# Optimization experiments

Hardware: AMD Instinct MI355X
Metric: run time of the kernel (lower is better)

The kernel has to match this reference:

```python
import jax, jax.numpy as jnp
from jax import lax
import numpy as np

LRELU_SLOPE = 0.1
DILATIONS = (1, 2, 4)
B, C, T = 8, 256, 8192


def pd_indexing(x, d, dilation):
    """Pitch-dependent past/future gather along time.
    x: (B, C, T); d: (B, 1, T) float dilation factors.
    Returns xP, xF: (B, C, T), zero where index is out of range.
    """
    b, c, t_len = x.shape
    t = jnp.arange(t_len, dtype=x.dtype)  # (T,)
    dil = d[:, 0, :] * dilation           # (B, T)
    idxP = jnp.round(t[None, :] - dil).astype(jnp.int32)  # (B, T)
    idxF = jnp.round(t[None, :] + dil).astype(jnp.int32)  # (B, T)
    validP = (idxP >= 0).astype(x.dtype)[:, None, :]        # (B,1,T)
    validF = (idxF < t_len).astype(x.dtype)[:, None, :]
    idxPc = jnp.broadcast_to(jnp.clip(idxP, 0, t_len - 1)[:, None, :], (b, c, t_len))
    idxFc = jnp.broadcast_to(jnp.clip(idxF, 0, t_len - 1)[:, None, :], (b, c, t_len))
    xP = jnp.take_along_axis(x, idxPc, axis=2) * validP
    xF = jnp.take_along_axis(x, idxFc, axis=2) * validF
    return xP, xF


def conv1x1(x, w, bias):
    # x: (B,C,T), w: (O,C), bias: (O,)
    return jnp.einsum('oc,bct->bot', w, x) + bias[None, :, None]


def conv3(x, w, bias):
    # x: (B,C,T), w: (O,C,3), padding=1
    y = lax.conv_general_dilated(x, w, window_strides=(1,), padding=[(1, 1)],
                                 dimension_numbers=('NCH', 'OIH', 'NCH'))
    return y + bias[None, :, None]


def setup_inputs() -> dict:
    key = jax.random.key(0)
    ks = jax.random.split(key, 8)
    x = jax.random.normal(ks[0], (B, C, T), dtype=jnp.float32)
    d = jax.random.uniform(ks[1], (B, 1, T), dtype=jnp.float32, minval=0.0, maxval=16.0)
    n = len(DILATIONS)
    s1 = 1.0 / np.sqrt(C)
    s3 = 1.0 / np.sqrt(3 * C)
    WC = jax.random.normal(ks[2], (n, C, C), dtype=jnp.float32) * s1
    WP = jax.random.normal(ks[3], (n, C, C), dtype=jnp.float32) * s1
    WF = jax.random.normal(ks[4], (n, C, C), dtype=jnp.float32) * s1
    WA = jax.random.normal(ks[5], (n, C, C, 3), dtype=jnp.float32) * s3
    bC = jnp.zeros((n, C), dtype=jnp.float32)
    bP = jnp.zeros((n, C), dtype=jnp.float32)
    bF = jnp.zeros((n, C), dtype=jnp.float32)
    bA = jnp.zeros((n, C), dtype=jnp.float32)
    return {"x": x, "d": d, "WC": WC, "bC": bC, "WP": WP, "bP": bP,
            "WF": WF, "bF": bF, "WA": WA, "bA": bA}


def reference(x, d, WC, bC, WP, bP, WF, bF, WA, bA):
    for i, dilation in enumerate(DILATIONS):
        xt = jax.nn.leaky_relu(x, LRELU_SLOPE)
        xP, xF = pd_indexing(xt, d, dilation)
        xt = conv1x1(xt, WC[i], bC[i]) + conv1x1(xP, WP[i], bP[i]) + conv1x1(xF, WF[i], bF[i])
        xt = jax.nn.leaky_relu(xt, LRELU_SLOPE)
        xt = conv3(xt, WA[i], bA[i])
        x = xt + x
    return x
```

## Files before the change

### kernel.cpp

```cpp
#include <hip/hip_runtime.h>
#include <hip/hip_bf16.h>
#include <cstddef>
#include <cstdint>

constexpr int Bn = 8, Cn = 256, Tn = 8192;
constexpr int NL = 3;
constexpr int Kc = 768;
constexpr float SLOPE = 0.1f;

typedef unsigned short u16;
using bf8   = __attribute__((ext_vector_type(8))) short;
using f32x4 = __attribute__((ext_vector_type(4))) float;

__device__ __forceinline__ float lrelu(float v) { return v > 0.f ? v : SLOPE * v; }
__device__ __forceinline__ u16 f2bf(float f) {
    __hip_bfloat16 h = __float2bfloat16(f);
    return *reinterpret_cast<u16*>(&h);
}

__device__ __forceinline__ void g2l16(const u16* g, u16* l) {
    __builtin_amdgcn_global_load_lds(
        (const __attribute__((address_space(1))) char*)g,
        (__attribute__((address_space(3))) char*)l, 16, 0, 0);
}

__global__ __launch_bounds__(256)
void k_wprep(const float* __restrict__ WC, const float* __restrict__ WP,
             const float* __restrict__ WF, const float* __restrict__ WA,
             const float* __restrict__ bC, const float* __restrict__ bP,
             const float* __restrict__ bF,
             u16* __restrict__ Wcat, u16* __restrict__ WAp, float* __restrict__ bSum,
             u16* __restrict__ zrow)
{
    if (blockIdx.x == 0) zrow[threadIdx.x] = 0;
    const int n1 = NL * Cn * Kc;
    for (int i = blockIdx.x * blockDim.x + threadIdx.x; i < n1;
         i += gridDim.x * blockDim.x) {
        int c = i % Cn;
        int s = (i / Cn) % 3;
        int o = (i / (3 * Cn)) % Cn;
        int l = i / (3 * Cn * Cn);
        size_t src = ((size_t)l * Cn + o) * Cn + c;
        float wc = (s == 0) ? WC[src] : (s == 1) ? WP[src] : WF[src];
        Wcat[i] = f2bf(wc);
        WAp[i] = f2bf(WA[src * 3 + s]);
    }
    for (int i = blockIdx.x * blockDim.x + threadIdx.x; i < NL * Cn;
         i += gridDim.x * blockDim.x)
        bSum[i] = bC[i] + bP[i] + bF[i];
}

__global__ __launch_bounds__(256)
void k_prep(const float* __restrict__ x, u16* __restrict__ xT)
{
    __shared__ float s[64][65];
    const int b = blockIdx.z, c0 = blockIdx.y * 64, t0 = blockIdx.x * 64;
    const int tid = threadIdx.x;
    const float* xb = x + ((size_t)b * Cn + c0) * Tn + t0;

    int tt = tid & 63, c4 = tid >> 6;
    for (int cc = c4; cc < 64; cc += 4)
        s[cc][tt] = xb[(size_t)cc * Tn + tt];
    __syncthreads();

    int ccS = tid & 63, t4 = tid >> 6;
    u16* xTb = xT + ((size_t)b * Tn + t0) * Cn + c0;
    for (int t2 = t4; t2 < 64; t2 += 4)
        xTb[(size_t)t2 * Cn + ccS] = f2bf(lrelu(s[ccS][t2]));
}

__global__ __launch_bounds__(256)
void k_gemm1(const u16* __restrict__ xT, const float* __restrict__ d,
             const u16* __restrict__ Wl, const float* __restrict__ bS,
             float dil, u16* __restrict__ zT, const u16* __restrict__ zrow)
{
    __shared__ u16 sX[128 * 32];
    __shared__ u16 sW[128 * 32];
    __shared__ int sRow[3][128];

    const int tid = threadIdx.x;
    const int b = blockIdx.z;
    const int t0 = blockIdx.x * 128;
    const int o0 = blockIdx.y * 128;

    if (tid < 128) {
        int t = t0 + tid;
        float dv = d[(size_t)b * Tn + t] * dil;
        int ip = (int)rintf((float)t - dv);
        int iF = (int)rintf((float)t + dv);
        sRow[0][tid] = t;
        sRow[1][tid] = (ip >= 0) ? ip : -1;
        sRow[2][tid] = (iF < Tn) ? iF : -1;
    }
    __syncthreads();

    const int srow = tid >> 2;
    const int schunk = (tid & 3) * 8;
    const u16* xTb = xT + (size_t)b * Tn * Cn;

    const u16 *pr0[3], *pr1[3];
    #pragma unroll
    for (int s = 0; s < 3; ++s) {
        int r0 = sRow[s][srow], r1 = sRow[s][srow + 64];
        pr0[s] = (r0 >= 0) ? (xTb + (size_t)r0 * Cn + schunk) : (zrow + schunk);
        pr1[s] = (r1 >= 0) ? (xTb + (size_t)r1 * Cn + schunk) : (zrow + schunk);
    }

    const int lane = tid & 63, wv = tid >> 6;
    const int wm = (wv & 1) * 64;
    const int wn = (wv >> 1) * 64;
    const int lr = lane & 15, quad = lane >> 4;

    f32x4 acc[4][4] = {};

    #pragma unroll
    for (int seg = 0; seg < 3; ++seg) {
        const u16* xr0 = pr0[seg];
        const u16* xr1 = pr1[seg];
        const u16* wp0 = Wl + (size_t)(o0 + srow) * Kc + seg * 256 + schunk;
        const u16* wp1 = wp0 + (size_t)64 * Kc;
        #pragma unroll
        for (int kk = 0; kk < 256; kk += 32) {
            __syncthreads();
            g2l16(wp0 + kk, sW + srow * 32 + schunk);
            g2l16(wp1 + kk, sW + (srow + 64) * 32 + schunk);
            g2l16(xr0 + kk, sX + srow * 32 + schunk);
            g2l16(xr1 + kk, sX + (srow + 64) * 32 + schunk);
            __syncthreads();

            bf8 af[4], bg[4];
            #pragma unroll
            for (int mi = 0; mi < 4; ++mi)
                af[mi] = *(const bf8*)(sX + (wm + mi * 16 + lr) * 32 + quad * 8);
            #pragma unroll
            for (int ni = 0; ni < 4; ++ni)
                bg[ni] = *(const bf8*)(sW + (wn + ni * 16 + lr) * 32 + quad * 8);
            #pragma unroll
            for (int mi = 0; mi < 4; ++mi)
                #pragma unroll
                for (int ni = 0; ni < 4; ++ni)
                    acc[mi][ni] = __builtin_amdgcn_mfma_f32_16x16x32_bf16(
                        af[mi], bg[ni], acc[mi][ni], 0, 0, 0);
        }
    }

    float bias[4];
    #pragma unroll
    for (int ni = 0; ni < 4; ++ni) bias[ni] = bS[o0 + wn + ni * 16 + lr];
    u16* zTb = zT + (size_t)b * Tn * Cn;
    #pragma unroll
    for (int mi = 0; mi < 4; ++mi)
        #pragma unroll
        for (int r = 0; r < 4; ++r) {
            int t = t0 + wm + mi * 16 + quad * 4 + r;
            u16* row = zTb + (size_t)t * Cn + o0 + wn;
            #pragma unroll
            for (int ni = 0; ni < 4; ++ni)
                row[ni * 16 + lr] = f2bf(lrelu(acc[mi][ni][r] + bias[ni]));
        }
}

__global__ __launch_bounds__(256)
void k_gemm2(const u16* __restrict__ zT, const u16* __restrict__ WAl,
             const float* __restrict__ bA, const float* __restrict__ xres,
             float* __restrict__ out, u16* __restrict__ xTn, int writeXT,
             const u16* __restrict__ zrow)
{
    __shared__ u16 smem[128 * 32 * 2];
    u16* sZ = smem;
    u16* sW = smem + 4096;

    const int tid = threadIdx.x;
    const int b = blockIdx.z;
    const int t0 = blockIdx.x * 128;
    const int o0 = blockIdx.y * 128;

    const int srow = tid >> 2;
    const int schunk = (tid & 3) * 8;
    const int lane = tid & 63, wv = tid >> 6;
    const int wo = (wv & 1) * 64;
    const int wt = (wv >> 1) * 64;
    const int lr = lane & 15, quad = lane >> 4;

    f32x4 acc[4][4] = {};
    const u16* zTb = zT + (size_t)b * Tn * Cn;

    #pragma unroll
    for (int tap = 0; tap < 3; ++tap) {
        const int r0 = t0 + srow + tap - 1;
        const int r1 = r0 + 64;
        const u16* zr0 = (r0 >= 0 && r0 < Tn) ? (zTb + (size_t)r0 * Cn + schunk)
                                              : (zrow + schunk);
        const u16* zr1 = (r1 >= 0 && r1 < Tn) ? (zTb + (size_t)r1 * Cn + schunk)
                                              : (zrow + schunk);
        const u16* wp0 = WAl + (size_t)(o0 + srow) * Kc + tap * 256 + schunk;
        const u16* wp1 = wp0 + (size_t)64 * Kc;
        #pragma unroll
        for (int kk = 0; kk < 256; kk += 32) {
            __syncthreads();
            g2l16(wp0 + kk, sW + srow * 32 + schunk);
            g2l16(wp1 + kk, sW + (srow + 64) * 32 + schunk);
            g2l16(zr0 + kk, sZ + srow * 32 + schunk);
            g2l16(zr1 + kk, sZ + (srow + 64) * 32 + schunk);
            __syncthreads();

            bf8 af[4], bg[4];
            #pragma unroll
            for (int mi = 0; mi < 4; ++mi)
                af[mi] = *(const bf8*)(sW + (wo + mi * 16 + lr) * 32 + quad * 8);
            #pragma unroll
            for (int ni = 0; ni < 4; ++ni)
                bg[ni] = *(const bf8*)(sZ + (wt + ni * 16 + lr) * 32 + quad * 8);
            #pragma unroll
            for (int mi = 0; mi < 4; ++mi)
                #pragma unroll
                for (int ni = 0; ni < 4; ++ni)
                    acc[mi][ni] = __builtin_amdgcn_mfma_f32_16x16x32_bf16(
                        af[mi], bg[ni], acc[mi][ni], 0, 0, 0);
        }
    }

    float biasv[4][4];
    #pragma unroll
    for (int mi = 0; mi < 4; ++mi) {
        float4 bb = *(const float4*)(bA + o0 + wo + mi * 16 + quad * 4);
        biasv[mi][0] = bb.x; biasv[mi][1] = bb.y; biasv[mi][2] = bb.z; biasv[mi][3] = bb.w;
    }

    if (writeXT) {
        u16* strip = smem + wv * 1152;
        u16* xTb2 = xTn + (size_t)b * Tn * Cn;
        #pragma unroll
        for (int ni = 0; ni < 4; ++ni) {
            __syncthreads();
            #pragma unroll
            for (int mi = 0; mi < 4; ++mi) {
                ushort4 pk;
                #pragma unroll
                for (int r = 0; r < 4; ++r) {
                    int o = o0 + wo + mi * 16 + quad * 4 + r;
                    size_t idx = ((size_t)b * Cn + o) * Tn + t0 + wt + ni * 16 + lr;
                    float v = acc[mi][ni][r] + biasv[mi][r] + xres[idx];
                    out[idx] = v;
                    ((u16*)&pk)[r] = f2bf(lrelu(v));
                }
                *(ushort4*)(strip + lr * 72 + mi * 16 + quad * 4) = pk;
            }
            __syncthreads();
            #pragma unroll
            for (int it = 0; it < 2; ++it) {
                int tt = (lane >> 3) + it * 8;
                uint4 vv = *(const uint4*)(strip + tt * 72 + (lane & 7) * 8);
                *(uint4*)(xTb2 + (size_t)(t0 + wt + ni * 16 + tt) * Cn
                          + o0 + wo + (lane & 7) * 8) = vv;
            }
        }
    } else {
        #pragma unroll
        for (int mi = 0; mi < 4; ++mi)
            #pragma unroll
            for (int r = 0; r < 4; ++r) {
                int o = o0 + wo + mi * 16 + quad * 4 + r;
                size_t base = ((size_t)b * Cn + o) * Tn + t0 + wt;
                #pragma unroll
                for (int ni = 0; ni < 4; ++ni) {
                    size_t idx = base + ni * 16 + lr;
                    out[idx] = acc[mi][ni][r] + biasv[mi][r] + xres[idx];
                }
            }
    }
}

extern "C" void kernel_launch(void* const* d_in, const int* in_sizes, int n_in,
                              void* d_out, int out_size, void* d_ws, size_t ws_size,
                              hipStream_t stream)
{
    const float* x  = (const float*)d_in[0];
    const float* d  = (const float*)d_in[1];
    const float* WC = (const float*)d_in[2];
    const float* bC = (const float*)d_in[3];
    const float* WP = (const float*)d_in[4];
    const float* bP = (const float*)d_in[5];
    const float* WF = (const float*)d_in[6];
    const float* bF = (const float*)d_in[7];
    const float* WA = (const float*)d_in[8];
    const float* bA = (const float*)d_in[9];
    float* out = (float*)d_out;

    char* ws = (char*)d_ws;
    u16*   xT   = (u16*)(ws);
    u16*   zT   = (u16*)(ws + (size_t)Bn * Tn * Cn * 2);
    u16*   Wcat = (u16*)(ws + (size_t)2 * Bn * Tn * Cn * 2);
    u16*   WAp  = Wcat + (size_t)NL * Cn * Kc;
    float* bSum = (float*)(WAp + (size_t)NL * Cn * Kc);
    u16*   zrow = (u16*)(bSum + NL * Cn);

    k_wprep<<<dim3(1024), dim3(256), 0, stream>>>(WC, WP, WF, WA, bC, bP, bF,
                                                  Wcat, WAp, bSum, zrow);

    dim3 gP(Tn / 64, Cn / 64, Bn);
    dim3 gG(Tn / 128, Cn / 128, Bn);
    dim3 blk(256);

    k_prep<<<gP, blk, 0, stream>>>(x, xT);

    const float dils[NL] = {1.f, 2.f, 4.f};
    const float* xcur = x;
    for (int i = 0; i < NL; ++i) {
        k_gemm1<<<gG, blk, 0, stream>>>(xT, d,
                                        Wcat + (size_t)i * Cn * Kc,
                                        bSum + (size_t)i * Cn,
                                        dils[i], zT, zrow);
        k_gemm2<<<gG, blk, 0, stream>>>(zT,
                                        WAp + (size_t)i * Cn * Kc,
                                        bA + (size_t)i * Cn,
                                        xcur, out, xT, (i < NL - 1) ? 1 : 0,
                                        zrow);
        xcur = out;
    }
}
```

Before: 418.3 us.

## Double-buffer LDS tiles in both GEMM kernels with one barrier per k-step

Both GEMM kernels now keep two LDS buffers for the activation and weight tiles. Each step issues the global-to-LDS DMA for the next k-slice before running the MFMAs on the current one, and the two barriers per step become one. This is meant to hide global load latency behind matrix math and cut synchronization overhead. In exchange, LDS per block doubles, which may lower occupancy, and the overlap only happens if the compiler does not insert a full vmcnt wait before the LDS reads.

```diff
diff --git a/kernel.cpp b/kernel.cpp
--- a/kernel.cpp
+++ b/kernel.cpp
@@ -74,8 +74,7 @@
              const u16* __restrict__ Wl, const float* __restrict__ bS,
              float dil, u16* __restrict__ zT, const u16* __restrict__ zrow)
 {
-    __shared__ u16 sX[128 * 32];
-    __shared__ u16 sW[128 * 32];
+    __shared__ u16 smem[4 * 4096];
     __shared__ int sRow[3][128];
 
     const int tid = threadIdx.x;
@@ -105,43 +104,49 @@
         pr0[s] = (r0 >= 0) ? (xTb + (size_t)r0 * Cn + schunk) : (zrow + schunk);
         pr1[s] = (r1 >= 0) ? (xTb + (size_t)r1 * Cn + schunk) : (zrow + schunk);
     }
+    const u16* wbase = Wl + (size_t)(o0 + srow) * Kc + schunk;
 
     const int lane = tid & 63, wv = tid >> 6;
     const int wm = (wv & 1) * 64;
     const int wn = (wv >> 1) * 64;
     const int lr = lane & 15, quad = lane >> 4;
 
+    const int ldsW = srow * 32 + schunk;
+    const int ldsW2 = (srow + 64) * 32 + schunk;
+
+    auto dma = [&](int kg, int bsel) {
+        int seg = kg >> 3, kk = (kg & 7) * 32;
+        u16* bx = smem + bsel * 4096;
+        u16* bw = smem + 8192 + bsel * 4096;
+        g2l16(wbase + seg * 256 + kk,                 bw + ldsW);
+        g2l16(wbase + (size_t)64 * Kc + seg * 256 + kk, bw + ldsW2);
+        g2l16(pr0[seg] + kk, bx + ldsW);
+        g2l16(pr1[seg] + kk, bx + ldsW2);
+    };
+
     f32x4 acc[4][4] = {};
-
-    #pragma unroll
-    for (int seg = 0; seg < 3; ++seg) {
-        const u16* xr0 = pr0[seg];
-        const u16* xr1 = pr1[seg];
-        const u16* wp0 = Wl + (size_t)(o0 + srow) * Kc + seg * 256 + schunk;
-        const u16* wp1 = wp0 + (size_t)64 * Kc;
-        #pragma unroll
-        for (int kk = 0; kk < 256; kk += 32) {
-            __syncthreads();
-            g2l16(wp0 + kk, sW + srow * 32 + schunk);
-            g2l16(wp1 + kk, sW + (srow + 64) * 32 + schunk);
-            g2l16(xr0 + kk, sX + srow * 32 + schunk);
-            g2l16(xr1 + kk, sX + (srow + 64) * 32 + schunk);
-            __syncthreads();
-
-            bf8 af[4], bg[4];
-            #pragma unroll
-            for (int mi = 0; mi < 4; ++mi)
-                af[mi] = *(const bf8*)(sX + (wm + mi * 16 + lr) * 32 + quad * 8);
+    dma(0, 0);
+
+    #pragma unroll
+    for (int kg = 0; kg < 24; ++kg) {
+        __syncthreads();
+        if (kg + 1 < 24) dma(kg + 1, (kg + 1) & 1);
+        const u16* bX = smem + (kg & 1) * 4096;
+        const u16* bW = smem + 8192 + (kg & 1) * 4096;
+
+        bf8 af[4], bg[4];
+        #pragma unroll
+        for (int mi = 0; mi < 4; ++mi)
+            af[mi] = *(const bf8*)(bX + (wm + mi * 16 + lr) * 32 + quad * 8);
+        #pragma unroll
+        for (int ni = 0; ni < 4; ++ni)
+            bg[ni] = *(const bf8*)(bW + (wn + ni * 16 + lr) * 32 + quad * 8);
+        #pragma unroll
+        for (int mi = 0; mi < 4; ++mi)
             #pragma unroll
             for (int ni = 0; ni < 4; ++ni)
-                bg[ni] = *(const bf8*)(sW + (wn + ni * 16 + lr) * 32 + quad * 8);
-            #pragma unroll
-            for (int mi = 0; mi < 4; ++mi)
-                #pragma unroll
-                for (int ni = 0; ni < 4; ++ni)
-                    acc[mi][ni] = __builtin_amdgcn_mfma_f32_16x16x32_bf16(
-                        af[mi], bg[ni], acc[mi][ni], 0, 0, 0);
-        }
+                acc[mi][ni] = __builtin_amdgcn_mfma_f32_16x16x32_bf16(
+                    af[mi], bg[ni], acc[mi][ni], 0, 0, 0);
     }
 
     float bias[4];
@@ -166,9 +171,7 @@
              float* __restrict__ out, u16* __restrict__ xTn, int writeXT,
              const u16* __restrict__ zrow)
 {
-    __shared__ u16 smem[128 * 32 * 2];
-    u16* sZ = smem;
-    u16* sW = smem + 4096;
+    __shared__ u16 smem[4 * 4096];
 
     const int tid = threadIdx.x;
     const int b = blockIdx.z;
@@ -182,42 +185,55 @@
     const int wt = (wv >> 1) * 64;
     const int lr = lane & 15, quad = lane >> 4;
 
+    const u16* zTb = zT + (size_t)b * Tn * Cn;
+    const u16 *zr0[3], *zr1[3];
+    #pragma unroll
+    for (int tap = 0; tap < 3; ++tap) {
+        int r0 = t0 + srow + tap - 1;
+        int r1 = r0 + 64;
+        zr0[tap] = (r0 >= 0 && r0 < Tn) ? (zTb + (size_t)r0 * Cn + schunk)
+                                        : (zrow + schunk);
+        zr1[tap] = (r1 >= 0 && r1 < Tn) ? (zTb + (size_t)r1 * Cn + schunk)
+                                        : (zrow + schunk);
+    }
+    const u16* wbase = WAl + (size_t)(o0 + srow) * Kc + schunk;
+
+    const int ldsW = srow * 32 + schunk;
+    const int ldsW2 = (srow + 64) * 32 + schunk;
+
+    auto dma = [&](int kg, int bsel) {
+        int tap = kg >> 3, kk = (kg & 7) * 32;
+        u16* bz = smem + bsel * 4096;
+        u16* bw = smem + 8192 + bsel * 4096;
+        g2l16(wbase + tap * 256 + kk,                   bw + ldsW);
+        g2l16(wbase + (size_t)64 * Kc + tap * 256 + kk, bw + ldsW2);
+        g2l16(zr0[tap] + kk, bz + ldsW);
+        g2l16(zr1[tap] + kk, bz + ldsW2);
+    };
+
     f32x4 acc[4][4] = {};
-    const u16* zTb = zT + (size_t)b * Tn * Cn;
-
-    #pragma unroll
-    for (int tap = 0; tap < 3; ++tap) {
-        const int r0 = t0 + srow + tap - 1;
-        const int r1 = r0 + 64;
-        const u16* zr0 = (r0 >= 0 && r0 < Tn) ? (zTb + (size_t)r0 * Cn + schunk)
-                                              : (zrow + schunk);
-        const u16* zr1 = (r1 >= 0 && r1 < Tn) ? (zTb + (size_t)r1 * Cn + schunk)
-                                              : (zrow + schunk);
-        const u16* wp0 = WAl + (size_t)(o0 + srow) * Kc + tap * 256 + schunk;
-        const u16* wp1 = wp0 + (size_t)64 * Kc;
-        #pragma unroll
-        for (int kk = 0; kk < 256; kk += 32) {
-            __syncthreads();
-            g2l16(wp0 + kk, sW + srow * 32 + schunk);
-            g2l16(wp1 + kk, sW + (srow + 64) * 32 + schunk);
-            g2l16(zr0 + kk, sZ + srow * 32 + schunk);
-            g2l16(zr1 + kk, sZ + (srow + 64) * 32 + schunk);
-            __syncthreads();
-
-            bf8 af[4], bg[4];
-            #pragma unroll
-            for (int mi = 0; mi < 4; ++mi)
-                af[mi] = *(const bf8*)(sW + (wo + mi * 16 + lr) * 32 + quad * 8);
+    dma(0, 0);
+
+    #pragma unroll
+    for (int kg = 0; kg < 24; ++kg) {
+        __syncthreads();
+        if (kg + 1 < 24) dma(kg + 1, (kg + 1) & 1);
+        const u16* bZ = smem + (kg & 1) * 4096;
+        const u16* bW = smem + 8192 + (kg & 1) * 4096;
+
+        bf8 af[4], bg[4];
+        #pragma unroll
+        for (int mi = 0; mi < 4; ++mi)
+            af[mi] = *(const bf8*)(bW + (wo + mi * 16 + lr) * 32 + quad * 8);
+        #pragma unroll
+        for (int ni = 0; ni < 4; ++ni)
+            bg[ni] = *(const bf8*)(bZ + (wt + ni * 16 + lr) * 32 + quad * 8);
+        #pragma unroll
+        for (int mi = 0; mi < 4; ++mi)
             #pragma unroll
             for (int ni = 0; ni < 4; ++ni)
-                bg[ni] = *(const bf8*)(sZ + (wt + ni * 16 + lr) * 32 + quad * 8);
-            #pragma unroll
-            for (int mi = 0; mi < 4; ++mi)
-                #pragma unroll
-                for (int ni = 0; ni < 4; ++ni)
-                    acc[mi][ni] = __builtin_amdgcn_mfma_f32_16x16x32_bf16(
-                        af[mi], bg[ni], acc[mi][ni], 0, 0, 0);
-        }
+                acc[mi][ni] = __builtin_amdgcn_mfma_f32_16x16x32_bf16(
+                    af[mi], bg[ni], acc[mi][ni], 0, 0, 0);
     }
 
     float biasv[4][4];
```

New measurement: 400.3 us. 4.3% less time.

## Stage activations through padded LDS with register prefetch; read weights from global

Applied to the files above, without the earlier changes.

Both GEMM kernels stop staging weight tiles in LDS. Each wave now loads its weight fragments straight from global memory into registers. Activation tiles are prefetched into registers one K-step ahead and then stored into a padded LDS tile (row stride 40) instead of going through global_load_lds. This aims to overlap global loads with MFMA work, halve LDS traffic and cut bank conflicts. The cost is duplicated weight fetches across waves and global reads that are less coalesced.

```diff
diff --git a/kernel.cpp b/kernel.cpp
--- a/kernel.cpp
+++ b/kernel.cpp
@@ -7,6 +7,7 @@
 constexpr int NL = 3;
 constexpr int Kc = 768;
 constexpr float SLOPE = 0.1f;
+constexpr int LP = 40;
 
 typedef unsigned short u16;
 using bf8   = __attribute__((ext_vector_type(8))) short;
@@ -16,12 +17,6 @@
 __device__ __forceinline__ u16 f2bf(float f) {
     __hip_bfloat16 h = __float2bfloat16(f);
     return *reinterpret_cast<u16*>(&h);
-}
-
-__device__ __forceinline__ void g2l16(const u16* g, u16* l) {
-    __builtin_amdgcn_global_load_lds(
-        (const __attribute__((address_space(1))) char*)g,
-        (__attribute__((address_space(3))) char*)l, 16, 0, 0);
 }
 
 __global__ __launch_bounds__(256)
@@ -74,8 +69,7 @@
              const u16* __restrict__ Wl, const float* __restrict__ bS,
              float dil, u16* __restrict__ zT, const u16* __restrict__ zrow)
 {
-    __shared__ u16 sX[128 * 32];
-    __shared__ u16 sW[128 * 32];
+    __shared__ u16 sX[128 * LP];
     __shared__ int sRow[3][128];
 
     const int tid = threadIdx.x;
@@ -111,37 +105,41 @@
     const int wn = (wv >> 1) * 64;
     const int lr = lane & 15, quad = lane >> 4;
 
+    const u16* wrow[4];
+    #pragma unroll
+    for (int ni = 0; ni < 4; ++ni)
+        wrow[ni] = Wl + (size_t)(o0 + wn + ni * 16 + lr) * Kc + quad * 8;
+
     f32x4 acc[4][4] = {};
-
-    #pragma unroll
-    for (int seg = 0; seg < 3; ++seg) {
-        const u16* xr0 = pr0[seg];
-        const u16* xr1 = pr1[seg];
-        const u16* wp0 = Wl + (size_t)(o0 + srow) * Kc + seg * 256 + schunk;
-        const u16* wp1 = wp0 + (size_t)64 * Kc;
-        #pragma unroll
-        for (int kk = 0; kk < 256; kk += 32) {
-            __syncthreads();
-            g2l16(wp0 + kk, sW + srow * 32 + schunk);
-            g2l16(wp1 + kk, sW + (srow + 64) * 32 + schunk);
-            g2l16(xr0 + kk, sX + srow * 32 + schunk);
-            g2l16(xr1 + kk, sX + (srow + 64) * 32 + schunk);
-            __syncthreads();
-
-            bf8 af[4], bg[4];
-            #pragma unroll
-            for (int mi = 0; mi < 4; ++mi)
-                af[mi] = *(const bf8*)(sX + (wm + mi * 16 + lr) * 32 + quad * 8);
+    uint4 xa = *(const uint4*)pr0[0];
+    uint4 xb2 = *(const uint4*)pr1[0];
+
+    #pragma unroll
+    for (int kg = 0; kg < 24; ++kg) {
+        __syncthreads();
+        *(uint4*)(sX + srow * LP + schunk) = xa;
+        *(uint4*)(sX + (srow + 64) * LP + schunk) = xb2;
+        bf8 bg[4];
+        #pragma unroll
+        for (int ni = 0; ni < 4; ++ni)
+            bg[ni] = *(const bf8*)(wrow[ni] + kg * 32);
+        if (kg < 23) {
+            int seg = (kg + 1) >> 3, off = ((kg + 1) & 7) * 32;
+            xa  = *(const uint4*)(pr0[seg] + off);
+            xb2 = *(const uint4*)(pr1[seg] + off);
+        }
+        __syncthreads();
+
+        bf8 af[4];
+        #pragma unroll
+        for (int mi = 0; mi < 4; ++mi)
+            af[mi] = *(const bf8*)(sX + (wm + mi * 16 + lr) * LP + quad * 8);
+        #pragma unroll
+        for (int mi = 0; mi < 4; ++mi)
             #pragma unroll
             for (int ni = 0; ni < 4; ++ni)
-                bg[ni] = *(const bf8*)(sW + (wn + ni * 16 + lr) * 32 + quad * 8);
-            #pragma unroll
-            for (int mi = 0; mi < 4; ++mi)
-                #pragma unroll
-                for (int ni = 0; ni < 4; ++ni)
-                    acc[mi][ni] = __builtin_amdgcn_mfma_f32_16x16x32_bf16(
-                        af[mi], bg[ni], acc[mi][ni], 0, 0, 0);
-        }
+                acc[mi][ni] = __builtin_amdgcn_mfma_f32_16x16x32_bf16(
+                    af[mi], bg[ni], acc[mi][ni], 0, 0, 0);
     }
 
     float bias[4];
@@ -166,9 +164,7 @@
              float* __restrict__ out, u16* __restrict__ xTn, int writeXT,
              const u16* __restrict__ zrow)
 {
-    __shared__ u16 smem[128 * 32 * 2];
-    u16* sZ = smem;
-    u16* sW = smem + 4096;
+    __shared__ u16 sZ[128 * LP];
 
     const int tid = threadIdx.x;
     const int b = blockIdx.z;
@@ -182,42 +178,53 @@
     const int wt = (wv >> 1) * 64;
     const int lr = lane & 15, quad = lane >> 4;
 
+    const u16* zTb = zT + (size_t)b * Tn * Cn;
+    const u16 *zr0[3], *zr1[3];
+    #pragma unroll
+    for (int tap = 0; tap < 3; ++tap) {
+        int r0 = t0 + srow + tap - 1;
+        int r1 = r0 + 64;
+        zr0[tap] = (r0 >= 0 && r0 < Tn) ? (zTb + (size_t)r0 * Cn + schunk)
+                                        : (zrow + schunk);
+        zr1[tap] = (r1 >= 0 && r1 < Tn) ? (zTb + (size_t)r1 * Cn + schunk)
+                                        : (zrow + schunk);
+    }
+
+    const u16* wrow[4];
+    #pragma unroll
+    for (int mi = 0; mi < 4; ++mi)
+        wrow[mi] = WAl + (size_t)(o0 + wo + mi * 16 + lr) * Kc + quad * 8;
+
     f32x4 acc[4][4] = {};
-    const u16* zTb = zT + (size_t)b * Tn * Cn;
-
-    #pragma unroll
-    for (int tap = 0; tap < 3; ++tap) {
-        const int r0 = t0 + srow + tap - 1;
-        const int r1 = r0 + 64;
-        const u16* zr0 = (r0 >= 0 && r0 < Tn) ? (zTb + (size_t)r0 * Cn + schunk)
-                                              : (zrow + schunk);
-        const u16* zr1 = (r1 >= 0 && r1 < Tn) ? (zTb + (size_t)r1 * Cn + schunk)
-                                              : (zrow + schunk);
-        const u16* wp0 = WAl + (size_t)(o0 + srow) * Kc + tap * 256 + schunk;
-        const u16* wp1 = wp0 + (size_t)64 * Kc;
-        #pragma unroll
-        for (int kk = 0; kk < 256; kk += 32) {
-            __syncthreads();
-            g2l16(wp0 + kk, sW + srow * 32 + schunk);
-            g2l16(wp1 + kk, sW + (srow + 64) * 32 + schunk);
-            g2l16(zr0 + kk, sZ + srow * 32 + schunk);
-            g2l16(zr1 + kk, sZ + (srow + 64) * 32 + schunk);
-            __syncthreads();
-
-            bf8 af[4], bg[4];
-            #pragma unroll
-            for (int mi = 0; mi < 4; ++mi)
-                af[mi] = *(const bf8*)(sW + (wo + mi * 16 + lr) * 32 + quad * 8);
+    uint4 za = *(const uint4*)zr0[0];
+    uint4 zb2 = *(const uint4*)zr1[0];
+
+    #pragma unroll
+    for (int kg = 0; kg < 24; ++kg) {
+        __syncthreads();
+        *(uint4*)(sZ + srow * LP + schunk) = za;
+        *(uint4*)(sZ + (srow + 64) * LP + schunk) = zb2;
+        bf8 af[4];
+        #pragma unroll
+        for (int mi = 0; mi < 4; ++mi)
+            af[mi] = *(const bf8*)(wrow[mi] + kg * 32);
+        if (kg < 23) {
+            int tap = (kg + 1) >> 3, off = ((kg + 1) & 7) * 32;
+            za  = *(const uint4*)(zr0[tap] + off);
+            zb2 = *(const uint4*)(zr1[tap] + off);
+        }
+        __syncthreads();
+
+        bf8 bg[4];
+        #pragma unroll
+        for (int ni = 0; ni < 4; ++ni)
+            bg[ni] = *(const bf8*)(sZ + (wt + ni * 16 + lr) * LP + quad * 8);
+        #pragma unroll
+        for (int mi = 0; mi < 4; ++mi)
             #pragma unroll
             for (int ni = 0; ni < 4; ++ni)
-                bg[ni] = *(const bf8*)(sZ + (wt + ni * 16 + lr) * 32 + quad * 8);
-            #pragma unroll
-            for (int mi = 0; mi < 4; ++mi)
-                #pragma unroll
-                for (int ni = 0; ni < 4; ++ni)
-                    acc[mi][ni] = __builtin_amdgcn_mfma_f32_16x16x32_bf16(
-                        af[mi], bg[ni], acc[mi][ni], 0, 0, 0);
-        }
+                acc[mi][ni] = __builtin_amdgcn_mfma_f32_16x16x32_bf16(
+                    af[mi], bg[ni], acc[mi][ni], 0, 0, 0);
     }
 
     float biasv[4][4];
@@ -228,7 +235,7 @@
     }
 
     if (writeXT) {
-        u16* strip = smem + wv * 1152;
+        u16* strip = sZ + wv * 1152;
         u16* xTb2 = xTn + (size_t)b * Tn * Cn;
         #pragma unroll
         for (int ni = 0; ni < 4; ++ni) {
```

After: 508.6 us. 1.22x slower.
